# Optimization experiments

Hardware: AMD Instinct MI355X
Metric: run time of the kernel (lower is better)

The kernel has to match this reference:

```python
import jax, jax.numpy as jnp
import numpy as np
import math

B, S, D, H, DFF, L = 256, 100, 512, 8, 2048, 4
HD = D // H
EPS = 1e-5


def _ln(x, g, b):
    mu = jnp.mean(x, axis=-1, keepdims=True)
    var = jnp.mean(jnp.square(x - mu), axis=-1, keepdims=True)
    return (x - mu) * jax.lax.rsqrt(var + EPS) * g + b


def setup_inputs() -> dict:
    key = jax.random.key(0)
    ks = jax.random.split(key, 16)
    sc = 0.02
    # contiguous valid-prefix mask: row b has `length[b]` ones then zeros
    lengths = jax.random.randint(ks[0], (B,), 1, S + 1)
    inputs = (jnp.arange(S)[None, :] < lengths[:, None]).astype(jnp.int32)
    inputs_emb = jax.random.normal(ks[1], (B, S, D), jnp.float32)
    return {
        "inputs": inputs,
        "inputs_emb": inputs_emb,
        "in_proj_w": jax.random.normal(ks[2], (L, 3 * D, D), jnp.float32) * sc,
        "in_proj_b": jnp.zeros((L, 3 * D), jnp.float32),
        "out_proj_w": jax.random.normal(ks[3], (L, D, D), jnp.float32) * sc,
        "out_proj_b": jnp.zeros((L, D), jnp.float32),
        "lin1_w": jax.random.normal(ks[4], (L, DFF, D), jnp.float32) * sc,
        "lin1_b": jnp.zeros((L, DFF), jnp.float32),
        "lin2_w": jax.random.normal(ks[5], (L, D, DFF), jnp.float32) * sc,
        "lin2_b": jnp.zeros((L, D), jnp.float32),
        "ln1_w": jnp.ones((L, D), jnp.float32),
        "ln1_b": jnp.zeros((L, D), jnp.float32),
        "ln2_w": jnp.ones((L, D), jnp.float32),
        "ln2_b": jnp.zeros((L, D), jnp.float32),
        "attn_w": jax.random.normal(ks[6], (D, 2 * D), jnp.float32) * sc,
        "attn_b": jnp.zeros((D,), jnp.float32),
    }


def reference(inputs, inputs_emb, in_proj_w, in_proj_b, out_proj_w, out_proj_b,
              lin1_w, lin1_b, lin2_w, lin2_b, ln1_w, ln1_b, ln2_w, ln2_b,
              attn_w, attn_b):
    # --- PosEmbedding (note: original uses a LINEAR div_term, no exp; faithful) ---
    pos = jnp.arange(S, dtype=jnp.float32)[:, None]                      # [S,1]
    div = jnp.arange(0, D, 2, dtype=jnp.float32) * (-math.log(100.0) / D)
    pe = jnp.zeros((S, D), jnp.float32)
    pe = pe.at[:, 0::2].set(jnp.sin(pos * div)).at[:, 1::2].set(jnp.cos(pos * div))
    x = inputs_emb + pe[None, :, :]                                       # [B,S,D]

    key_pad = (inputs == 0)                                               # [B,S]
    bias = jnp.where(key_pad[:, None, None, :], -jnp.inf, 0.0)            # [B,1,1,S]

    # --- post-norm TransformerEncoderLayer stack (relu FFN, dropout off) ---
    for i in range(L):
        qkv = x @ in_proj_w[i].T + in_proj_b[i]                           # [B,S,3D]
        q, k, v = jnp.split(qkv, 3, axis=-1)
        q = q.reshape(B, S, H, HD).transpose(0, 2, 1, 3)                  # [B,H,S,HD]
        k = k.reshape(B, S, H, HD).transpose(0, 2, 1, 3)
        v = v.reshape(B, S, H, HD).transpose(0, 2, 1, 3)
        scores = jnp.einsum('bhqd,bhkd->bhqk', q, k) / math.sqrt(HD) + bias
        p = jax.nn.softmax(scores, axis=-1)
        attn = jnp.einsum('bhqk,bhkd->bhqd', p, v)
        attn = attn.transpose(0, 2, 1, 3).reshape(B, S, D)
        attn = attn @ out_proj_w[i].T + out_proj_b[i]
        x = _ln(x + attn, ln1_w[i], ln1_b[i])
        ff = jax.nn.relu(x @ lin1_w[i].T + lin1_b[i]) @ lin2_w[i].T + lin2_b[i]
        x = _ln(x + ff, ln2_w[i], ln2_b[i])

    # --- per-sample ragged attention pooling, vectorized via masking ---
    # score[b,s] = sum_d Linear([cur_q_b ; x_bs]); softmax over valid prefix
    cur_q = x[:, -1]                                                      # [B,D]
    W1, W2 = attn_w[:, :D], attn_w[:, D:]                                 # each [D,D]
    s_q = (cur_q @ W1.T + attn_b).sum(-1)                                 # [B]
    s_v = (x @ W2.T).sum(-1)                                              # [B,S]
    scores = jnp.where(key_pad, -jnp.inf, s_q[:, None] + s_v)             # [B,S]
    p = jax.nn.softmax(scores, axis=-1)
    out = jnp.einsum('bs,bsd->bd', p, x)[:, None, :]                      # [B,1,D]
    return out
```

## Files before the change

kernel.cpp:

```cpp
#include <hip/hip_runtime.h>
#include <math.h>

#define NB 256
#define NS 100
#define ND 512
#define NH 8
#define NDFF 2048
#define NL 4
#define NM (NB * NS)

typedef unsigned short u16;
typedef unsigned short u16x4 __attribute__((ext_vector_type(4)));
typedef unsigned short u16x8 __attribute__((ext_vector_type(8)));
typedef __bf16 bf16x8 __attribute__((ext_vector_type(8)));
typedef float f32x4 __attribute__((ext_vector_type(4)));
typedef _Float16 f16x2 __attribute__((ext_vector_type(2)));
typedef _Float16 f16x8 __attribute__((ext_vector_type(8)));

#if __has_builtin(__builtin_amdgcn_fdot2)
#define USE_FDOT2 1
#else
#define USE_FDOT2 0
#endif

__device__ __forceinline__ float b2f(u16 u) {
  unsigned v = ((unsigned)u) << 16;
  return __builtin_bit_cast(float, v);
}
__device__ __forceinline__ u16 f2b(float f) {
  unsigned u = __builtin_bit_cast(unsigned, f);
  u += 0x7fffu + ((u >> 16) & 1u);
  return (u16)(u >> 16);
}
__device__ __forceinline__ void gload_lds16(const void* g, void* l) {
  __builtin_amdgcn_global_load_lds(
      (const __attribute__((address_space(1))) unsigned int*)g,
      (__attribute__((address_space(3))) unsigned int*)l, 16, 0, 0);
}

__global__ __launch_bounds__(256) void cast_kernel(const float* __restrict__ in,
                                                   u16* __restrict__ out) {
  int i = blockIdx.x * 256 + threadIdx.x;
  float4 v = ((const float4*)in)[i];
  u16x4 o = {f2b(v.x), f2b(v.y), f2b(v.z), f2b(v.w)};
  ((u16x4*)out)[i] = o;
}

__global__ __launch_bounds__(256) void scan_kernel(const int* __restrict__ mask,
                                                   int* __restrict__ offs,
                                                   int* __restrict__ meta,
                                                   int BC, int NC) {
  const int b = threadIdx.x;
  const int* mp = mask + b * NS;
  int len = 0;
#pragma unroll
  for (int i = 0; i < NS; i += 4) {
    int4 v = *(const int4*)(mp + i);
    len += v.x + v.y + v.z + v.w;
  }
  int v = len;
#pragma unroll
  for (int off = 1; off < 64; off <<= 1) {
    int u = __shfl_up(v, off);
    if ((b & 63) >= off) v += u;
  }
  __shared__ int wsum[4];
  __shared__ int incl[256];
  if ((b & 63) == 63) wsum[b >> 6] = v;
  __syncthreads();
  int add = 0;
  for (int w = 0; w < (b >> 6); ++w) add += wsum[w];
  v += add;
  incl[b] = v;
  __syncthreads();
  offs[b + 1] = v;
  if (b == 0) offs[0] = 0;
  if (b < NC) meta[b] = incl[(b + 1) * BC - 1] - (b ? incl[b * BC - 1] : 0);
}

__global__ __launch_bounds__(128) void pe_compact_kernel(const float* __restrict__ emb,
                                                         const int* __restrict__ offs,
                                                         int BC,
                                                         float* __restrict__ x,
                                                         u16* __restrict__ xb) {
  const int tok = blockIdx.x;
  const int b = tok / NS, s = tok - b * NS;
  const int ob = offs[b];
  const int len = offs[b + 1] - ob;
  if (s >= len) return;
  const int c = b / BC;
  const size_t dst = ((size_t)c * BC * NS + (ob - offs[c * BC]) + s) * ND;
  const int t = threadIdx.x;
  const int d0 = t * 4;
  float4 ev = *(const float4*)(emb + (size_t)tok * ND + d0);
  float o[4];
#pragma unroll
  for (int e = 0; e < 4; ++e) {
    int d = d0 + e;
    float ang = (float)s * (float)(d & ~1) * (-4.6051701859880914f / (float)ND);
    float pe = (d & 1) ? __cosf(ang) : __sinf(ang);
    o[e] = ((const float*)&ev)[e] + pe;
  }
  *(float4*)(x + dst + d0) = (float4){o[0], o[1], o[2], o[3]};
  u16x4 ob16 = {f2b(o[0]), f2b(o[1]), f2b(o[2]), f2b(o[3])};
  *(u16x4*)(xb + dst + d0) = ob16;
}

template <int TM, bool RELU, bool OUTBF16, bool RESID>
__global__ __launch_bounds__(256) void gemm_mfma(const u16* __restrict__ A,
                                                 const u16* __restrict__ W,
                                                 const float* __restrict__ bias,
                                                 const float* __restrict__ R,
                                                 float* __restrict__ Cf,
                                                 u16* __restrict__ Cb,
                                                 const int* __restrict__ pMr,
                                                 int N, int K) {
  constexpr int MF = TM / 32;
  const int m0 = blockIdx.y * TM, n0 = blockIdx.x * 128;
  if (m0 >= ((*pMr + TM - 1) & ~(TM - 1))) return;
  __shared__ u16 As[TM * 64];
  __shared__ u16 Ws[128 * 64];
  const int t = threadIdx.x;
  const int lane = t & 63;
  const int wave = t >> 6;
  const int wr = wave >> 1, wc = wave & 1;
  const int srow = lane >> 3;
  const int sblk = (lane & 7) ^ srow;
  const u16* gA = A + (size_t)(m0 + wave * 8 + srow) * K + sblk * 8;
  const u16* gW = W + (size_t)(n0 + wave * 8 + srow) * K + sblk * 8;
  u16* lA = As + wave * 512;
  u16* lW = Ws + wave * 512;
  f32x4 acc[MF][4];
#pragma unroll
  for (int m = 0; m < MF; ++m)
#pragma unroll
    for (int n = 0; n < 4; ++n) acc[m][n] = (f32x4){0.f, 0.f, 0.f, 0.f};
  const int lg = lane >> 4;
  const int li = lane & 15;
  const int l7 = li & 7;
  for (int k0 = 0; k0 < K; k0 += 64) {
    __syncthreads();
#pragma unroll
    for (int i = 0; i < MF; ++i)
      gload_lds16(gA + k0 + (size_t)(32 * i) * K, lA + i * 2048);
#pragma unroll
    for (int i = 0; i < 4; ++i)
      gload_lds16(gW + k0 + (size_t)(32 * i) * K, lW + i * 2048);
    __syncthreads();
#pragma unroll
    for (int h = 0; h < 2; ++h) {
      bf16x8 af[MF], bf_[4];
#pragma unroll
      for (int m = 0; m < MF; ++m) {
        int row = wr * (16 * MF) + m * 16 + li;
        af[m] = __builtin_bit_cast(
            bf16x8, *(const u16x8*)&As[row * 64 + (((h << 2) + lg) ^ l7) * 8]);
      }
#pragma unroll
      for (int n = 0; n < 4; ++n) {
        int row = wc * 64 + n * 16 + li;
        bf_[n] = __builtin_bit_cast(
            bf16x8, *(const u16x8*)&Ws[row * 64 + (((h << 2) + lg) ^ l7) * 8]);
      }
#pragma unroll
      for (int m = 0; m < MF; ++m)
#pragma unroll
        for (int n = 0; n < 4; ++n)
          acc[m][n] = __builtin_amdgcn_mfma_f32_16x16x32_bf16(af[m], bf_[n], acc[m][n], 0, 0, 0);
    }
  }
#pragma unroll
  for (int m = 0; m < MF; ++m) {
    int row = m0 + wr * (16 * MF) + m * 16 + lg * 4;
#pragma unroll
    for (int n = 0; n < 4; ++n) {
      int col = n0 + wc * 64 + n * 16 + li;
      float bv = bias[col];
#pragma unroll
      for (int j = 0; j < 4; ++j) {
        float v = acc[m][n][j] + bv;
        if (RESID) v += R[(size_t)(row + j) * N + col];
        if (RELU) v = fmaxf(v, 0.f);
        if (OUTBF16) Cb[(size_t)(row + j) * N + col] = f2b(v);
        else Cf[(size_t)(row + j) * N + col] = v;
      }
    }
  }
}

__global__ __launch_bounds__(128) void attn_kernel(const u16* __restrict__ qkv,
                                                   const int* __restrict__ offs,
                                                   int bBase,
                                                   u16* __restrict__ out) {
  const int bh = blockIdx.x;
  const int bl = bh >> 3, h = bh & 7;
  const int bg = bBase + bl;
  const int ob = offs[bg] - offs[bBase];
  const int len = offs[bg + 1] - offs[bg];
  __shared__ u16 Ksb[NS * 64];
  __shared__ float Vs[NS * 64];
  const int t = threadIdx.x;
  const u16* base = qkv + (size_t)ob * 1536 + h * 64;

  for (int e = t; e < len * 16; e += 128) {
    int s = e >> 4, d4 = (e & 15) << 2;
    u16x4 kk = *(const u16x4*)(base + (size_t)s * 1536 + 512 + d4);
#if USE_FDOT2
    u16x4 kh;
#pragma unroll
    for (int q = 0; q < 4; ++q) {
      _Float16 hv = (_Float16)b2f(kk[q]);
      kh[q] = __builtin_bit_cast(u16, hv);
    }
    *(u16x4*)&Ksb[s * 64 + d4] = kh;
#else
    *(u16x4*)&Ksb[s * 64 + d4] = kk;
#endif
    u16x4 vv = *(const u16x4*)(base + (size_t)s * 1536 + 1024 + d4);
    Vs[s * 64 + d4 + 0] = b2f(vv[0]);
    Vs[s * 64 + d4 + 1] = b2f(vv[1]);
    Vs[s * 64 + d4 + 2] = b2f(vv[2]);
    Vs[s * 64 + d4 + 3] = b2f(vv[3]);
  }

#if USE_FDOT2
  f16x2 qh[32];
#else
  float qf[64];
#endif
  if (t < len) {
    const u16* gq = base + (size_t)t * 1536;
#pragma unroll
    for (int j = 0; j < 8; ++j) {
      u16x8 qq = *(const u16x8*)(gq + j * 8);
#if USE_FDOT2
#pragma unroll
      for (int e = 0; e < 4; ++e) {
        f16x2 p;
        p[0] = (_Float16)b2f(qq[e * 2 + 0]);
        p[1] = (_Float16)b2f(qq[e * 2 + 1]);
        qh[j * 4 + e] = p;
      }
#else
#pragma unroll
      for (int e = 0; e < 8; ++e) qf[j * 8 + e] = b2f(qq[e]) * 0.125f;
#endif
    }
  }
  __syncthreads();
  if (t >= len) return;

  f32x4 acc[16];
#pragma unroll
  for (int dq = 0; dq < 16; ++dq) acc[dq] = (f32x4){0.f, 0.f, 0.f, 0.f};
  float m = -INFINITY, sum = 0.f;

  int s = 0;
  for (; s + 2 <= len; s += 2) {
    float a0 = 0.f, a1 = 0.f, a2 = 0.f, a3 = 0.f;
    float c0 = 0.f, c1 = 0.f, c2 = 0.f, c3 = 0.f;
#if USE_FDOT2
#pragma unroll
    for (int j = 0; j < 8; ++j) {
      f16x8 ka = __builtin_bit_cast(f16x8, *(const u16x8*)&Ksb[s * 64 + j * 8]);
      f16x8 kb = __builtin_bit_cast(f16x8, *(const u16x8*)&Ksb[(s + 1) * 64 + j * 8]);
      f16x2 ka0 = {ka[0], ka[1]}, ka1 = {ka[2], ka[3]};
      f16x2 ka2 = {ka[4], ka[5]}, ka3 = {ka[6], ka[7]};
      f16x2 kb0 = {kb[0], kb[1]}, kb1 = {kb[2], kb[3]};
      f16x2 kb2 = {kb[4], kb[5]}, kb3 = {kb[6], kb[7]};
      a0 = __builtin_amdgcn_fdot2(qh[j * 4 + 0], ka0, a0, false);
      c0 = __builtin_amdgcn_fdot2(qh[j * 4 + 0], kb0, c0, false);
      a1 = __builtin_amdgcn_fdot2(qh[j * 4 + 1], ka1, a1, false);
      c1 = __builtin_amdgcn_fdot2(qh[j * 4 + 1], kb1, c1, false);
      a2 = __builtin_amdgcn_fdot2(qh[j * 4 + 2], ka2, a2, false);
      c2 = __builtin_amdgcn_fdot2(qh[j * 4 + 2], kb2, c2, false);
      a3 = __builtin_amdgcn_fdot2(qh[j * 4 + 3], ka3, a3, false);
      c3 = __builtin_amdgcn_fdot2(qh[j * 4 + 3], kb3, c3, false);
    }
    float a = ((a0 + a1) + (a2 + a3)) * 0.125f;
    float c = ((c0 + c1) + (c2 + c3)) * 0.125f;
#else
#pragma unroll
    for (int j = 0; j < 8; ++j) {
      u16x8 ka = *(const u16x8*)&Ksb[s * 64 + j * 8];
      u16x8 kb = *(const u16x8*)&Ksb[(s + 1) * 64 + j * 8];
      a0 += qf[j * 8 + 0] * b2f(ka[0]); c0 += qf[j * 8 + 0] * b2f(kb[0]);
      a1 += qf[j * 8 + 1] * b2f(ka[1]); c1 += qf[j * 8 + 1] * b2f(kb[1]);
      a2 += qf[j * 8 + 2] * b2f(ka[2]); c2 += qf[j * 8 + 2] * b2f(kb[2]);
      a3 += qf[j * 8 + 3] * b2f(ka[3]); c3 += qf[j * 8 + 3] * b2f(kb[3]);
      a0 += qf[j * 8 + 4] * b2f(ka[4]); c0 += qf[j * 8 + 4] * b2f(kb[4]);
      a1 += qf[j * 8 + 5] * b2f(ka[5]); c1 += qf[j * 8 + 5] * b2f(kb[5]);
      a2 += qf[j * 8 + 6] * b2f(ka[6]); c2 += qf[j * 8 + 6] * b2f(kb[6]);
      a3 += qf[j * 8 + 7] * b2f(ka[7]); c3 += qf[j * 8 + 7] * b2f(kb[7]);
    }
    float a = (a0 + a1) + (a2 + a3);
    float c = (c0 + c1) + (c2 + c3);
#endif
    float mx2 = fmaxf(a, c);
    if (mx2 > m + 8.f) {
      float cs = __expf(m - mx2);
      sum *= cs;
#pragma unroll
      for (int dq = 0; dq < 16; ++dq) acc[dq] *= cs;
      m = mx2;
    }
    float pa = __expf(a - m);
    float pc = __expf(c - m);
    sum += pa + pc;
#pragma unroll
    for (int dq = 0; dq < 16; ++dq) {
      f32x4 va = *(const f32x4*)&Vs[s * 64 + dq * 4];
      f32x4 vb = *(const f32x4*)&Vs[(s + 1) * 64 + dq * 4];
      acc[dq] += pa * va + pc * vb;
    }
  }
  if (s < len) {
    float a0 = 0.f, a1 = 0.f, a2 = 0.f, a3 = 0.f;
#if USE_FDOT2
#pragma unroll
    for (int j = 0; j < 8; ++j) {
      f16x8 ka = __builtin_bit_cast(f16x8, *(const u16x8*)&Ksb[s * 64 + j * 8]);
      f16x2 ka0 = {ka[0], ka[1]}, ka1 = {ka[2], ka[3]};
      f16x2 ka2 = {ka[4], ka[5]}, ka3 = {ka[6], ka[7]};
      a0 = __builtin_amdgcn_fdot2(qh[j * 4 + 0], ka0, a0, false);
      a1 = __builtin_amdgcn_fdot2(qh[j * 4 + 1], ka1, a1, false);
      a2 = __builtin_amdgcn_fdot2(qh[j * 4 + 2], ka2, a2, false);
      a3 = __builtin_amdgcn_fdot2(qh[j * 4 + 3], ka3, a3, false);
    }
    float a = ((a0 + a1) + (a2 + a3)) * 0.125f;
#else
#pragma unroll
    for (int j = 0; j < 8; ++j) {
      u16x8 ka = *(const u16x8*)&Ksb[s * 64 + j * 8];
      a0 += qf[j * 8 + 0] * b2f(ka[0]);
      a1 += qf[j * 8 + 1] * b2f(ka[1]);
      a2 += qf[j * 8 + 2] * b2f(ka[2]);
      a3 += qf[j * 8 + 3] * b2f(ka[3]);
      a0 += qf[j * 8 + 4] * b2f(ka[4]);
      a1 += qf[j * 8 + 5] * b2f(ka[5]);
      a2 += qf[j * 8 + 6] * b2f(ka[6]);
      a3 += qf[j * 8 + 7] * b2f(ka[7]);
    }
    float a = (a0 + a1) + (a2 + a3);
#endif
    if (a > m + 8.f) {
      float cs = __expf(m - a);
      sum *= cs;
#pragma unroll
      for (int dq = 0; dq < 16; ++dq) acc[dq] *= cs;
      m = a;
    }
    float p = __expf(a - m);
    sum += p;
#pragma unroll
    for (int dq = 0; dq < 16; ++dq)
      acc[dq] += p * *(const f32x4*)&Vs[s * 64 + dq * 4];
  }

  float inv = 1.f / sum;
  u16* op = out + (size_t)(ob + t) * ND + h * 64;
#pragma unroll
  for (int j = 0; j < 8; ++j) {
    u16x8 o;
#pragma unroll
    for (int e = 0; e < 8; ++e) {
      int d = j * 8 + e;
      o[e] = f2b(acc[d >> 2][d & 3] * inv);
    }
    *(u16x8*)(op + j * 8) = o;
  }
}

__global__ __launch_bounds__(128) void add_ln_kernel(float* __restrict__ x,
                                                     u16* __restrict__ xb,
                                                     const float* __restrict__ g,
                                                     const float* __restrict__ bb,
                                                     const int* __restrict__ pMr) {
  const int row = blockIdx.x;
  if (row >= *pMr) return;
  const int t = threadIdx.x;
  const size_t base = (size_t)row * ND + t * 4;
  float4 v = *(const float4*)(x + base);
  float s = (v.x + v.y) + (v.z + v.w);
  float q = (v.x * v.x + v.y * v.y) + (v.z * v.z + v.w * v.w);
#pragma unroll
  for (int off = 32; off; off >>= 1) {
    s += __shfl_down(s, off);
    q += __shfl_down(q, off);
  }
  __shared__ float sb[4];
  const int wid = t >> 6;
  if ((t & 63) == 0) { sb[wid * 2] = s; sb[wid * 2 + 1] = q; }
  __syncthreads();
  float ts = sb[0] + sb[2];
  float tq = sb[1] + sb[3];
  float mean = ts * (1.f / (float)ND);
  float var = tq * (1.f / (float)ND) - mean * mean;
  float rstd = rsqrtf(var + 1e-5f);
  float4 gg = *(const float4*)(g + t * 4);
  float4 bv = *(const float4*)(bb + t * 4);
  float o0 = (v.x - mean) * rstd * gg.x + bv.x;
  float o1 = (v.y - mean) * rstd * gg.y + bv.y;
  float o2 = (v.z - mean) * rstd * gg.z + bv.z;
  float o3 = (v.w - mean) * rstd * gg.w + bv.w;
  *(float4*)(x + base) = (float4){o0, o1, o2, o3};
  u16x4 ob = {f2b(o0), f2b(o1), f2b(o2), f2b(o3)};
  *(u16x4*)(xb + base) = ob;
}

__global__ __launch_bounds__(64) void w2sum_kernel(const float* __restrict__ attn_w,
                                                   float* __restrict__ w2sum) {
  int d = blockIdx.x * 64 + threadIdx.x;
  float s = 0.f;
  for (int o = 0; o < ND; ++o) s += attn_w[(size_t)o * 1024 + 512 + d];
  w2sum[d] = s;
}

__global__ __launch_bounds__(256) void pool_kernel(const float* __restrict__ x,
                                                   const int* __restrict__ offs,
                                                   int BC,
                                                   const float* __restrict__ w2sum,
                                                   float* __restrict__ out) {
  const int b = blockIdx.x;
  const int c = b / BC;
  const int ob = offs[b] - offs[c * BC];
  const int len = offs[b + 1] - offs[b];
  const float* xr0 = x + ((size_t)c * BC * NS + ob) * ND;
  const int t = threadIdx.x;
  __shared__ float wsm[ND];
  __shared__ float sv[NS + 12];
  __shared__ float pv[256];
  __shared__ float red[8];
  wsm[t] = w2sum[t];
  wsm[t + 256] = w2sum[t + 256];
  __syncthreads();
  const int wv = t >> 6, ln = t & 63;
  for (int s = wv; s < len; s += 4) {
    const float* xr = xr0 + (size_t)s * ND;
    float acc = 0.f;
#pragma unroll
    for (int j = 0; j < 8; ++j) acc += xr[ln + j * 64] * wsm[ln + j * 64];
#pragma unroll
    for (int off = 32; off; off >>= 1) acc += __shfl_xor(acc, off);
    if (ln == 0) sv[s] = acc;
  }
  __syncthreads();
  float v = (t < len) ? sv[t] : -INFINITY;
  float m_ = v;
#pragma unroll
  for (int off = 32; off; off >>= 1) m_ = fmaxf(m_, __shfl_xor(m_, off));
  if (ln == 0) red[wv] = m_;
  __syncthreads();
  const float mx = fmaxf(fmaxf(red[0], red[1]), fmaxf(red[2], red[3]));
  float e = (t < len) ? __expf(v - mx) : 0.f;
  pv[t] = e;
  float s_ = e;
#pragma unroll
  for (int off = 32; off; off >>= 1) s_ += __shfl_xor(s_, off);
  if (ln == 0) red[4 + wv] = s_;
  __syncthreads();
  const float inv = 1.f / ((red[4] + red[5]) + (red[6] + red[7]));
  float a0 = 0.f, a1 = 0.f;
  for (int s = 0; s < len; ++s) {
    float p = pv[s];
    const float* xr = xr0 + (size_t)s * ND;
    a0 += p * xr[t];
    a1 += p * xr[t + 256];
  }
  out[(size_t)b * ND + t] = a0 * inv;
  out[(size_t)b * ND + t + 256] = a1 * inv;
}

extern "C" void kernel_launch(void* const* d_in, const int* in_sizes, int n_in,
                              void* d_out, int out_size, void* d_ws, size_t ws_size,
                              hipStream_t stream) {
  const int* mask = (const int*)d_in[0];
  const float* emb = (const float*)d_in[1];
  const float* in_proj_w = (const float*)d_in[2];
  const float* in_proj_b = (const float*)d_in[3];
  const float* out_proj_w = (const float*)d_in[4];
  const float* out_proj_b = (const float*)d_in[5];
  const float* lin1_w = (const float*)d_in[6];
  const float* lin1_b = (const float*)d_in[7];
  const float* lin2_w = (const float*)d_in[8];
  const float* lin2_b = (const float*)d_in[9];
  const float* ln1_w = (const float*)d_in[10];
  const float* ln1_b = (const float*)d_in[11];
  const float* ln2_w = (const float*)d_in[12];
  const float* ln2_b = (const float*)d_in[13];
  const float* attn_w = (const float*)d_in[14];

  char* wsb = (char*)d_ws;
  size_t off = 0;
  auto alloc = [&](size_t bytes) -> char* {
    char* p = wsb + off;
    off += (bytes + 255) & ~(size_t)255;
    return p;
  };
  float* x   = (float*)alloc((size_t)NM * ND * 4);
  u16* xb    = (u16*)alloc((size_t)NM * ND * 2);
  u16* wqkv  = (u16*)alloc((size_t)NL * 1536 * 512 * 2);
  u16* wout  = (u16*)alloc((size_t)NL * 512 * 512 * 2);
  u16* w1b   = (u16*)alloc((size_t)NL * 2048 * 512 * 2);
  u16* w2b   = (u16*)alloc((size_t)NL * 512 * 2048 * 2);
  float* w2s = (float*)alloc(ND * 4);
  int* offs  = (int*)alloc((NB + 1) * 4);
  int* meta  = (int*)alloc(16 * 4);
  size_t fixedEnd = off;

  int BC = 32;
  const int cands[4] = {256, 128, 64, 32};
  auto alup = [](size_t b) { return (b + 255) & ~(size_t)255; };
  for (int ci = 0; ci < 4; ++ci) {
    size_t Mc = (size_t)cands[ci] * NS;
    if (fixedEnd + alup(Mc * 2048 * 2) <= ws_size) { BC = cands[ci]; break; }
  }
  const size_t Mc = (size_t)BC * NS;
  const int NC = NB / BC;
  u16* big  = (u16*)alloc(Mc * 2048 * 2);
  u16* attO = big + Mc * 1536;

  cast_kernel<<<NL * 1536 * 512 / 1024, 256, 0, stream>>>(in_proj_w, wqkv);
  cast_kernel<<<NL * 512 * 512 / 1024, 256, 0, stream>>>(out_proj_w, wout);
  cast_kernel<<<NL * 2048 * 512 / 1024, 256, 0, stream>>>(lin1_w, w1b);
  cast_kernel<<<NL * 512 * 2048 / 1024, 256, 0, stream>>>(lin2_w, w2b);
  scan_kernel<<<1, 256, 0, stream>>>(mask, offs, meta, BC, NC);
  pe_compact_kernel<<<NM, 128, 0, stream>>>(emb, offs, BC, x, xb);

  for (int i = 0; i < NL; ++i) {
    for (int c = 0; c < NC; ++c) {
      float* xc = x + (size_t)c * Mc * ND;
      u16* xbc = xb + (size_t)c * Mc * ND;
      const int* pMr = meta + c;
      gemm_mfma<128, false, true, false><<<dim3(1536 / 128, Mc / 128), 256, 0, stream>>>(
          xbc, wqkv + (size_t)i * 1536 * 512, in_proj_b + i * 1536, nullptr, nullptr, big, pMr, 1536, 512);
      attn_kernel<<<BC * NH, 128, 0, stream>>>(big, offs, c * BC, attO);
      gemm_mfma<64, false, false, true><<<dim3(512 / 128, Mc / 64), 256, 0, stream>>>(
          attO, wout + (size_t)i * 512 * 512, out_proj_b + i * 512, xc, xc, nullptr, pMr, 512, 512);
      add_ln_kernel<<<Mc, 128, 0, stream>>>(xc, xbc, ln1_w + i * 512, ln1_b + i * 512, pMr);
      gemm_mfma<128, true, true, false><<<dim3(2048 / 128, Mc / 128), 256, 0, stream>>>(
          xbc, w1b + (size_t)i * 2048 * 512, lin1_b + i * 2048, nullptr, nullptr, big, pMr, 2048, 512);
      gemm_mfma<64, false, false, true><<<dim3(512 / 128, Mc / 64), 256, 0, stream>>>(
          big, w2b + (size_t)i * 512 * 2048, lin2_b + i * 512, xc, xc, nullptr, pMr, 512, 2048);
      add_ln_kernel<<<Mc, 128, 0, stream>>>(xc, xbc, ln2_w + i * 512, ln2_b + i * 512, pMr);
    }
  }

  w2sum_kernel<<<ND / 64, 64, 0, stream>>>(attn_w, w2s);
  pool_kernel<<<NB, 256, 0, stream>>>(x, offs, BC, w2s, (float*)d_out);
}
```

Before: 1.191 ms.

## Split attention over key halves with a separate merge kernel

Attention for each (batch, head) is split into two blocks, each handling half of the keys. Each block writes unnormalized bf16 partial outputs plus its running max and sum, and a merge kernel combines them with log-sum-exp rescaling. This doubles the number of attention blocks and halves each block's serial key loop and shared memory, aiming at better occupancy. In exchange it adds an extra kernel launch, extra global traffic for the partials, redundant Q loads, and bf16 rounding of the unnormalized partial accumulators.

```diff
diff --git a/kernel.cpp b/kernel.cpp
--- a/kernel.cpp
+++ b/kernel.cpp
@@ -188,6 +188,28 @@
   }
 }
 
+#if USE_FDOT2
+#define QREGS f16x2 qh[32]
+#define LOADQ(gq)                                   \
+  _Pragma("unroll") for (int j = 0; j < 8; ++j) {   \
+    u16x8 qq = *(const u16x8*)((gq) + j * 8);       \
+    _Pragma("unroll") for (int e = 0; e < 4; ++e) { \
+      f16x2 p;                                      \
+      p[0] = (_Float16)b2f(qq[e * 2 + 0]);          \
+      p[1] = (_Float16)b2f(qq[e * 2 + 1]);          \
+      qh[j * 4 + e] = p;                            \
+    }                                               \
+  }
+#else
+#define QREGS float qh[64]
+#define LOADQ(gq)                                   \
+  _Pragma("unroll") for (int j = 0; j < 8; ++j) {   \
+    u16x8 qq = *(const u16x8*)((gq) + j * 8);       \
+    _Pragma("unroll") for (int e = 0; e < 8; ++e)   \
+      qh[j * 8 + e] = b2f(qq[e]) * 0.125f;          \
+  }
+#endif
+
 __global__ __launch_bounds__(128) void attn_kernel(const u16* __restrict__ qkv,
                                                    const int* __restrict__ offs,
                                                    int bBase,
@@ -222,31 +244,8 @@
     Vs[s * 64 + d4 + 2] = b2f(vv[2]);
     Vs[s * 64 + d4 + 3] = b2f(vv[3]);
   }
-
-#if USE_FDOT2
-  f16x2 qh[32];
-#else
-  float qf[64];
-#endif
-  if (t < len) {
-    const u16* gq = base + (size_t)t * 1536;
-#pragma unroll
-    for (int j = 0; j < 8; ++j) {
-      u16x8 qq = *(const u16x8*)(gq + j * 8);
-#if USE_FDOT2
-#pragma unroll
-      for (int e = 0; e < 4; ++e) {
-        f16x2 p;
-        p[0] = (_Float16)b2f(qq[e * 2 + 0]);
-        p[1] = (_Float16)b2f(qq[e * 2 + 1]);
-        qh[j * 4 + e] = p;
-      }
-#else
-#pragma unroll
-      for (int e = 0; e < 8; ++e) qf[j * 8 + e] = b2f(qq[e]) * 0.125f;
-#endif
-    }
-  }
+  QREGS;
+  if (t < len) { LOADQ(base + (size_t)t * 1536); }
   __syncthreads();
   if (t >= len) return;
 
@@ -254,7 +253,6 @@
 #pragma unroll
   for (int dq = 0; dq < 16; ++dq) acc[dq] = (f32x4){0.f, 0.f, 0.f, 0.f};
   float m = -INFINITY, sum = 0.f;
-
   int s = 0;
   for (; s + 2 <= len; s += 2) {
     float a0 = 0.f, a1 = 0.f, a2 = 0.f, a3 = 0.f;
@@ -284,14 +282,14 @@
     for (int j = 0; j < 8; ++j) {
       u16x8 ka = *(const u16x8*)&Ksb[s * 64 + j * 8];
       u16x8 kb = *(const u16x8*)&Ksb[(s + 1) * 64 + j * 8];
-      a0 += qf[j * 8 + 0] * b2f(ka[0]); c0 += qf[j * 8 + 0] * b2f(kb[0]);
-      a1 += qf[j * 8 + 1] * b2f(ka[1]); c1 += qf[j * 8 + 1] * b2f(kb[1]);
-      a2 += qf[j * 8 + 2] * b2f(ka[2]); c2 += qf[j * 8 + 2] * b2f(kb[2]);
-      a3 += qf[j * 8 + 3] * b2f(ka[3]); c3 += qf[j * 8 + 3] * b2f(kb[3]);
-      a0 += qf[j * 8 + 4] * b2f(ka[4]); c0 += qf[j * 8 + 4] * b2f(kb[4]);
-      a1 += qf[j * 8 + 5] * b2f(ka[5]); c1 += qf[j * 8 + 5] * b2f(kb[5]);
-      a2 += qf[j * 8 + 6] * b2f(ka[6]); c2 += qf[j * 8 + 6] * b2f(kb[6]);
-      a3 += qf[j * 8 + 7] * b2f(ka[7]); c3 += qf[j * 8 + 7] * b2f(kb[7]);
+      a0 += qh[j * 8 + 0] * b2f(ka[0]); c0 += qh[j * 8 + 0] * b2f(kb[0]);
+      a1 += qh[j * 8 + 1] * b2f(ka[1]); c1 += qh[j * 8 + 1] * b2f(kb[1]);
+      a2 += qh[j * 8 + 2] * b2f(ka[2]); c2 += qh[j * 8 + 2] * b2f(kb[2]);
+      a3 += qh[j * 8 + 3] * b2f(ka[3]); c3 += qh[j * 8 + 3] * b2f(kb[3]);
+      a0 += qh[j * 8 + 4] * b2f(ka[4]); c0 += qh[j * 8 + 4] * b2f(kb[4]);
+      a1 += qh[j * 8 + 5] * b2f(ka[5]); c1 += qh[j * 8 + 5] * b2f(kb[5]);
+      a2 += qh[j * 8 + 6] * b2f(ka[6]); c2 += qh[j * 8 + 6] * b2f(kb[6]);
+      a3 += qh[j * 8 + 7] * b2f(ka[7]); c3 += qh[j * 8 + 7] * b2f(kb[7]);
     }
     float a = (a0 + a1) + (a2 + a3);
     float c = (c0 + c1) + (c2 + c3);
@@ -332,14 +330,14 @@
 #pragma unroll
     for (int j = 0; j < 8; ++j) {
       u16x8 ka = *(const u16x8*)&Ksb[s * 64 + j * 8];
-      a0 += qf[j * 8 + 0] * b2f(ka[0]);
-      a1 += qf[j * 8 + 1] * b2f(ka[1]);
-      a2 += qf[j * 8 + 2] * b2f(ka[2]);
-      a3 += qf[j * 8 + 3] * b2f(ka[3]);
-      a0 += qf[j * 8 + 4] * b2f(ka[4]);
-      a1 += qf[j * 8 + 5] * b2f(ka[5]);
-      a2 += qf[j * 8 + 6] * b2f(ka[6]);
-      a3 += qf[j * 8 + 7] * b2f(ka[7]);
+      a0 += qh[j * 8 + 0] * b2f(ka[0]);
+      a1 += qh[j * 8 + 1] * b2f(ka[1]);
+      a2 += qh[j * 8 + 2] * b2f(ka[2]);
+      a3 += qh[j * 8 + 3] * b2f(ka[3]);
+      a0 += qh[j * 8 + 4] * b2f(ka[4]);
+      a1 += qh[j * 8 + 5] * b2f(ka[5]);
+      a2 += qh[j * 8 + 6] * b2f(ka[6]);
+      a3 += qh[j * 8 + 7] * b2f(ka[7]);
     }
     float a = (a0 + a1) + (a2 + a3);
 #endif
@@ -356,7 +354,6 @@
     for (int dq = 0; dq < 16; ++dq)
       acc[dq] += p * *(const f32x4*)&Vs[s * 64 + dq * 4];
   }
-
   float inv = 1.f / sum;
   u16* op = out + (size_t)(ob + t) * ND + h * 64;
 #pragma unroll
@@ -369,6 +366,202 @@
     }
     *(u16x8*)(op + j * 8) = o;
   }
+}
+
+#define KHALF 50
+__global__ __launch_bounds__(128) void attn_split_kernel(const u16* __restrict__ qkv,
+                                                         const int* __restrict__ offs,
+                                                         int bBase, int Mc,
+                                                         u16* __restrict__ part0,
+                                                         u16* __restrict__ part1,
+                                                         float2* __restrict__ msum) {
+  const int bh = blockIdx.x;
+  const int side = blockIdx.y;
+  const int bl = bh >> 3, h = bh & 7;
+  const int bg = bBase + bl;
+  const int ob = offs[bg] - offs[bBase];
+  const int len = offs[bg + 1] - offs[bg];
+  const int hl = (len + 1) >> 1;
+  const int k0 = side ? hl : 0;
+  const int k1 = side ? len : hl;
+  const int nk = k1 - k0;
+  __shared__ u16 Ksb[KHALF * 64];
+  __shared__ float Vs[KHALF * 64];
+  const int t = threadIdx.x;
+  const u16* baseQ = qkv + (size_t)ob * 1536 + h * 64;
+  const u16* baseK = baseQ + (size_t)k0 * 1536;
+
+  for (int e = t; e < nk * 16; e += 128) {
+    int s = e >> 4, d4 = (e & 15) << 2;
+    u16x4 kk = *(const u16x4*)(baseK + (size_t)s * 1536 + 512 + d4);
+#if USE_FDOT2
+    u16x4 kh;
+#pragma unroll
+    for (int q = 0; q < 4; ++q) {
+      _Float16 hv = (_Float16)b2f(kk[q]);
+      kh[q] = __builtin_bit_cast(u16, hv);
+    }
+    *(u16x4*)&Ksb[s * 64 + d4] = kh;
+#else
+    *(u16x4*)&Ksb[s * 64 + d4] = kk;
+#endif
+    u16x4 vv = *(const u16x4*)(baseK + (size_t)s * 1536 + 1024 + d4);
+    Vs[s * 64 + d4 + 0] = b2f(vv[0]);
+    Vs[s * 64 + d4 + 1] = b2f(vv[1]);
+    Vs[s * 64 + d4 + 2] = b2f(vv[2]);
+    Vs[s * 64 + d4 + 3] = b2f(vv[3]);
+  }
+  QREGS;
+  if (t < len) { LOADQ(baseQ + (size_t)t * 1536); }
+  __syncthreads();
+  if (t >= len) return;
+
+  f32x4 acc[16];
+#pragma unroll
+  for (int dq = 0; dq < 16; ++dq) acc[dq] = (f32x4){0.f, 0.f, 0.f, 0.f};
+  float m = -INFINITY, sum = 0.f;
+  int s = 0;
+  for (; s + 2 <= nk; s += 2) {
+    float a0 = 0.f, a1 = 0.f, a2 = 0.f, a3 = 0.f;
+    float c0 = 0.f, c1 = 0.f, c2 = 0.f, c3 = 0.f;
+#if USE_FDOT2
+#pragma unroll
+    for (int j = 0; j < 8; ++j) {
+      f16x8 ka = __builtin_bit_cast(f16x8, *(const u16x8*)&Ksb[s * 64 + j * 8]);
+      f16x8 kb = __builtin_bit_cast(f16x8, *(const u16x8*)&Ksb[(s + 1) * 64 + j * 8]);
+      f16x2 ka0 = {ka[0], ka[1]}, ka1 = {ka[2], ka[3]};
+      f16x2 ka2 = {ka[4], ka[5]}, ka3 = {ka[6], ka[7]};
+      f16x2 kb0 = {kb[0], kb[1]}, kb1 = {kb[2], kb[3]};
+      f16x2 kb2 = {kb[4], kb[5]}, kb3 = {kb[6], kb[7]};
+      a0 = __builtin_amdgcn_fdot2(qh[j * 4 + 0], ka0, a0, false);
+      c0 = __builtin_amdgcn_fdot2(qh[j * 4 + 0], kb0, c0, false);
+      a1 = __builtin_amdgcn_fdot2(qh[j * 4 + 1], ka1, a1, false);
+      c1 = __builtin_amdgcn_fdot2(qh[j * 4 + 1], kb1, c1, false);
+      a2 = __builtin_amdgcn_fdot2(qh[j * 4 + 2], ka2, a2, false);
+      c2 = __builtin_amdgcn_fdot2(qh[j * 4 + 2], kb2, c2, false);
+      a3 = __builtin_amdgcn_fdot2(qh[j * 4 + 3], ka3, a3, false);
+      c3 = __builtin_amdgcn_fdot2(qh[j * 4 + 3], kb3, c3, false);
+    }
+    float a = ((a0 + a1) + (a2 + a3)) * 0.125f;
+    float c = ((c0 + c1) + (c2 + c3)) * 0.125f;
+#else
+#pragma unroll
+    for (int j = 0; j < 8; ++j) {
+      u16x8 ka = *(const u16x8*)&Ksb[s * 64 + j * 8];
+      u16x8 kb = *(const u16x8*)&Ksb[(s + 1) * 64 + j * 8];
+      a0 += qh[j * 8 + 0] * b2f(ka[0]); c0 += qh[j * 8 + 0] * b2f(kb[0]);
+      a1 += qh[j * 8 + 1] * b2f(ka[1]); c1 += qh[j * 8 + 1] * b2f(kb[1]);
+      a2 += qh[j * 8 + 2] * b2f(ka[2]); c2 += qh[j * 8 + 2] * b2f(kb[2]);
+      a3 += qh[j * 8 + 3] * b2f(ka[3]); c3 += qh[j * 8 + 3] * b2f(kb[3]);
+      a0 += qh[j * 8 + 4] * b2f(ka[4]); c0 += qh[j * 8 + 4] * b2f(kb[4]);
+      a1 += qh[j * 8 + 5] * b2f(ka[5]); c1 += qh[j * 8 + 5] * b2f(kb[5]);
+      a2 += qh[j * 8 + 6] * b2f(ka[6]); c2 += qh[j * 8 + 6] * b2f(kb[6]);
+      a3 += qh[j * 8 + 7] * b2f(ka[7]); c3 += qh[j * 8 + 7] * b2f(kb[7]);
+    }
+    float a = (a0 + a1) + (a2 + a3);
+    float c = (c0 + c1) + (c2 + c3);
+#endif
+    float mx2 = fmaxf(a, c);
+    if (mx2 > m + 8.f) {
+      float cs = __expf(m - mx2);
+      sum *= cs;
+#pragma unroll
+      for (int dq = 0; dq < 16; ++dq) acc[dq] *= cs;
+      m = mx2;
+    }
+    float pa = __expf(a - m);
+    float pc = __expf(c - m);
+    sum += pa + pc;
+#pragma unroll
+    for (int dq = 0; dq < 16; ++dq) {
+      f32x4 va = *(const f32x4*)&Vs[s * 64 + dq * 4];
+      f32x4 vb = *(const f32x4*)&Vs[(s + 1) * 64 + dq * 4];
+      acc[dq] += pa * va + pc * vb;
+    }
+  }
+  if (s < nk) {
+    float a0 = 0.f, a1 = 0.f, a2 = 0.f, a3 = 0.f;
+#if USE_FDOT2
+#pragma unroll
+    for (int j = 0; j < 8; ++j) {
+      f16x8 ka = __builtin_bit_cast(f16x8, *(const u16x8*)&Ksb[s * 64 + j * 8]);
+      f16x2 ka0 = {ka[0], ka[1]}, ka1 = {ka[2], ka[3]};
+      f16x2 ka2 = {ka[4], ka[5]}, ka3 = {ka[6], ka[7]};
+      a0 = __builtin_amdgcn_fdot2(qh[j * 4 + 0], ka0, a0, false);
+      a1 = __builtin_amdgcn_fdot2(qh[j * 4 + 1], ka1, a1, false);
+      a2 = __builtin_amdgcn_fdot2(qh[j * 4 + 2], ka2, a2, false);
+      a3 = __builtin_amdgcn_fdot2(qh[j * 4 + 3], ka3, a3, false);
+    }
+    float a = ((a0 + a1) + (a2 + a3)) * 0.125f;
+#else
+#pragma unroll
+    for (int j = 0; j < 8; ++j) {
+      u16x8 ka = *(const u16x8*)&Ksb[s * 64 + j * 8];
+      a0 += qh[j * 8 + 0] * b2f(ka[0]);
+      a1 += qh[j * 8 + 1] * b2f(ka[1]);
+      a2 += qh[j * 8 + 2] * b2f(ka[2]);
+      a3 += qh[j * 8 + 3] * b2f(ka[3]);
+      a0 += qh[j * 8 + 4] * b2f(ka[4]);
+      a1 += qh[j * 8 + 5] * b2f(ka[5]);
+      a2 += qh[j * 8 + 6] * b2f(ka[6]);
+      a3 += qh[j * 8 + 7] * b2f(ka[7]);
+    }
+    float a = (a0 + a1) + (a2 + a3);
+#endif
+    if (a > m + 8.f) {
+      float cs = __expf(m - a);
+      sum *= cs;
+#pragma unroll
+      for (int dq = 0; dq < 16; ++dq) acc[dq] *= cs;
+      m = a;
+    }
+    float p = __expf(a - m);
+    sum += p;
+#pragma unroll
+    for (int dq = 0; dq < 16; ++dq)
+      acc[dq] += p * *(const f32x4*)&Vs[s * 64 + dq * 4];
+  }
+
+  const int row = ob + t;
+  msum[((size_t)side * NH + h) * Mc + row] = (float2){m, sum};
+  u16* pp = (side ? part1 : part0) + (size_t)row * ND + h * 64;
+#pragma unroll
+  for (int j = 0; j < 8; ++j) {
+    u16x8 o;
+#pragma unroll
+    for (int e = 0; e < 8; ++e) {
+      int d = j * 8 + e;
+      o[e] = f2b(acc[d >> 2][d & 3]);
+    }
+    *(u16x8*)(pp + j * 8) = o;
+  }
+}
+
+__global__ __launch_bounds__(128) void attn_merge_kernel(u16* __restrict__ part0,
+                                                         const u16* __restrict__ part1,
+                                                         const float2* __restrict__ msum,
+                                                         const int* __restrict__ pMr,
+                                                         int Mc) {
+  const int r = blockIdx.x;
+  if (r >= *pMr) return;
+  const int t = threadIdx.x;
+  const int d0 = t * 4;
+  const int h = d0 >> 6;
+  float2 s0 = msum[(size_t)h * Mc + r];
+  float2 s1 = msum[((size_t)NH + h) * Mc + r];
+  float newm = fmaxf(s0.x, s1.x);
+  float cs0 = __expf(s0.x - newm);
+  float cs1 = __expf(s1.x - newm);
+  float inv = 1.f / (s0.y * cs0 + s1.y * cs1);
+  u16* p0 = part0 + (size_t)r * ND + d0;
+  const u16* p1 = part1 + (size_t)r * ND + d0;
+  u16x4 a = *(u16x4*)p0;
+  u16x4 b = *(const u16x4*)p1;
+  u16x4 o;
+#pragma unroll
+  for (int e = 0; e < 4; ++e)
+    o[e] = f2b((b2f(a[e]) * cs0 + b2f(b[e]) * cs1) * inv);
+  *(u16x4*)p0 = o;
 }
 
 __global__ __launch_bounds__(128) void add_ln_kernel(float* __restrict__ x,
@@ -520,6 +713,16 @@
   u16* big  = (u16*)alloc(Mc * 2048 * 2);
   u16* attO = big + Mc * 1536;
 
+  size_t needP1 = alup(Mc * 512 * 2);
+  size_t needMS = alup(2 * NH * Mc * 8);
+  bool splitOK = (off + needP1 + needMS <= ws_size);
+  u16* part1 = nullptr;
+  float2* msum = nullptr;
+  if (splitOK) {
+    part1 = (u16*)alloc(Mc * 512 * 2);
+    msum = (float2*)alloc(2 * NH * Mc * 8);
+  }
+
   cast_kernel<<<NL * 1536 * 512 / 1024, 256, 0, stream>>>(in_proj_w, wqkv);
   cast_kernel<<<NL * 512 * 512 / 1024, 256, 0, stream>>>(out_proj_w, wout);
   cast_kernel<<<NL * 2048 * 512 / 1024, 256, 0, stream>>>(lin1_w, w1b);
@@ -534,7 +737,13 @@
       const int* pMr = meta + c;
       gemm_mfma<128, false, true, false><<<dim3(1536 / 128, Mc / 128), 256, 0, stream>>>(
           xbc, wqkv + (size_t)i * 1536 * 512, in_proj_b + i * 1536, nullptr, nullptr, big, pMr, 1536, 512);
-      attn_kernel<<<BC * NH, 128, 0, stream>>>(big, offs, c * BC, attO);
+      if (splitOK) {
+        attn_split_kernel<<<dim3(BC * NH, 2), 128, 0, stream>>>(
+            big, offs, c * BC, (int)Mc, attO, part1, msum);
+        attn_merge_kernel<<<Mc, 128, 0, stream>>>(attO, part1, msum, pMr, (int)Mc);
+      } else {
+        attn_kernel<<<BC * NH, 128, 0, stream>>>(big, offs, c * BC, attO);
+      }
       gemm_mfma<64, false, false, true><<<dim3(512 / 128, Mc / 64), 256, 0, stream>>>(
           attO, wout + (size_t)i * 512 * 512, out_proj_b + i * 512, xc, xc, nullptr, pMr, 512, 512);
       add_ln_kernel<<<Mc, 128, 0, stream>>>(xc, xbc, ln1_w + i * 512, ln1_b + i * 512, pMr);
```

Measured after the change: 1.148 ms. 1.04x faster.
